# Optimization experiments

Measured on AMD Instinct MI355X. Metric: run time of the kernel, lower is better.

## Reference

```python
import jax, jax.numpy as jnp
import numpy as np

B, T, I, H, O = 1024, 512, 128, 256, 64


def setup_inputs() -> dict:
    key = jax.random.key(0)
    ks = jax.random.split(key, 12)
    def lin(k, shape, fan_in):
        return jax.random.uniform(k, shape, jnp.float32, -1.0, 1.0) / np.sqrt(fan_in)
    return {
        "x": jax.random.normal(ks[0], (B, T, I), jnp.float32),
        "h0": jnp.zeros((B, H), jnp.float32),
        # GRUCell params (gate order: r, z, n as in PyTorch)
        "W_ih": lin(ks[1], (3 * H, I), H),
        "b_ih": lin(ks[2], (3 * H,), H),
        "W_hh": lin(ks[3], (3 * H, H), H),
        "b_hh": lin(ks[4], (3 * H,), H),
        # input_transform Linear(I -> H)
        "Wt": lin(ks[5], (H, I), I),
        "bt": lin(ks[6], (H,), I),
        # output_proj Linear(H -> O)
        "Wo": lin(ks[7], (O, H), H),
        "bo": lin(ks[8], (O,), H),
        # gate_proj Linear(H -> O)
        "Wg": lin(ks[9], (O, H), H),
        "bg": lin(ks[10], (O,), H),
    }


def reference(x, h0, W_ih, b_ih, W_hh, b_hh, Wt, bt, Wo, bo, Wg, bg):
    # Precompute all input-side projections with big GEMMs (time-major for scan)
    xi = jnp.einsum("bti,gi->tbg", x, W_ih) + b_ih          # [T,B,3H]
    ti = jax.nn.silu(jnp.einsum("bti,hi->tbh", x, Wt) + bt)  # [T,B,H]

    def step(h, inp):
        xi_t, ti_t = inp
        hh = h @ W_hh.T + b_hh                               # [B,3H]
        xr, xz, xn = jnp.split(xi_t, 3, axis=-1)
        hr, hz, hn = jnp.split(hh, 3, axis=-1)
        r = jax.nn.sigmoid(xr + hr)
        z = jax.nn.sigmoid(xz + hz)
        n = jnp.tanh(xn + r * hn)
        h_new = (1.0 - z) * n + z * h
        proj = (h_new + ti_t) @ Wo.T + bo                    # [B,O]
        gate = jax.nn.sigmoid(h_new @ Wg.T + bg)             # [B,O]
        return h_new, proj * gate

    _, outs = jax.lax.scan(step, h0, (xi, ti))               # outs: [T,B,O]
    return jnp.mean(outs, axis=0)                            # [B,O]
```

## Files before the change

### kernel.cpp

```cpp
#include <hip/hip_runtime.h>
#include <hip/hip_bf16.h>


typedef __attribute__((ext_vector_type(8))) __bf16 bf16x8;
typedef __attribute__((ext_vector_type(4))) __bf16 bf16x4;
typedef __attribute__((ext_vector_type(4))) float f32x4;

#define MFMA(a, b, c) __builtin_amdgcn_mfma_f32_16x16x32_bf16(a, b, c, 0, 0, 0)

__device__ __forceinline__ float fsig(float v) {
  float e = __builtin_amdgcn_exp2f(v * -1.442695041f);
  return __builtin_amdgcn_rcpf(1.0f + e);
}
__device__ __forceinline__ float ftanh(float v) {
  float e = __builtin_amdgcn_exp2f(v * 2.885390082f);
  return 1.0f - 2.0f * __builtin_amdgcn_rcpf(1.0f + e);
}

#define O_WIN 0u
#define O_WHH 262144u
#define O_WO  655360u
#define O_WG  688128u
#define O_B1  720896u
#define O_H   724992u
#define O_ACC 1773568u
#define O_TIO 2035712u

__global__ void k1_prep(const float* __restrict__ Wih, const float* __restrict__ Wt,
                        const float* __restrict__ Whh, const float* __restrict__ Wo,
                        const float* __restrict__ Wg, const float* __restrict__ bih,
                        const float* __restrict__ bhh, const float* __restrict__ bt,
                        const float* __restrict__ h0, char* __restrict__ ws) {
  unsigned n = blockIdx.x * 256u + threadIdx.x;
  __bf16* win = (__bf16*)(ws + O_WIN);
  __bf16* whh = (__bf16*)(ws + O_WHH);
  __bf16* wo = (__bf16*)(ws + O_WO);
  __bf16* wg = (__bf16*)(ws + O_WG);
  float* b1 = (float*)(ws + O_B1);
  float* hb = (float*)(ws + O_H);
  float* ac = (float*)(ws + O_ACC);
  if (n < 98304u) win[n] = (__bf16)Wih[n];
  else if (n < 131072u) { unsigned i = n - 98304u; win[98304u + i] = (__bf16)Wt[i]; }
  else if (n < 327680u) { unsigned i = n - 131072u; whh[i] = (__bf16)Whh[i]; }
  else if (n < 344064u) { unsigned i = n - 327680u; wo[i] = (__bf16)Wo[i]; }
  else if (n < 360448u) { unsigned i = n - 344064u; wg[i] = (__bf16)Wg[i]; }
  else if (n < 361472u) {
    unsigned i = n - 360448u;
    float v = (i < 512u) ? (bih[i] + bhh[i]) : ((i < 768u) ? bih[i] : bt[i - 768u]);
    b1[i] = v;
  } else if (n < 623616u) { unsigned i = n - 361472u; hb[i] = h0[i]; }
  else if (n < 689152u) { unsigned i = n - 623616u; ac[i] = 0.0f; }
}

__global__ __launch_bounds__(256, 2) void k2_xi(
    const float* __restrict__ x, const __bf16* __restrict__ win,
    const float* __restrict__ b1, __bf16* __restrict__ xi, int t0, int tcbits) {
  extern __shared__ char sm2[];
  __bf16* Asm = (__bf16*)sm2;
  __bf16* Bsm = (__bf16*)(sm2 + 34816);
  const int tid = threadIdx.x;
  const int lane = tid & 63, wv = tid >> 6;
  const int m0 = blockIdx.x * 128;
  const int tcm = (1 << tcbits) - 1;
#pragma unroll
  for (int rnd = 0; rnd < 16; ++rnd) {
    int row = rnd * 8 + (tid >> 5);
    int cr = m0 + row;
    int bb = cr >> tcbits, tt = cr & tcm;
    const float* xr = x + ((size_t)bb * 512 + (size_t)(t0 + tt)) * 128 + (tid & 31) * 4;
    float4 v = *(const float4*)xr;
    bf16x4 b4 = {(__bf16)v.x, (__bf16)v.y, (__bf16)v.z, (__bf16)v.w};
    *(bf16x4*)&Asm[row * 136 + (tid & 31) * 4] = b4;
  }
  for (int nc = 0; nc < 6; ++nc) {
    __syncthreads();
#pragma unroll
    for (int rnd = 0; rnd < 8; ++rnd) {
      int rr = rnd * 16 + (tid >> 4);
      uint4 w4 = *(const uint4*)(win + (size_t)(nc * 128 + rr) * 128 + (tid & 15) * 8);
      *(uint4*)&Bsm[rr * 136 + (tid & 15) * 8] = w4;
    }
    __syncthreads();
    f32x4 zv = {0.f, 0.f, 0.f, 0.f};
    f32x4 acc[2][8];
#pragma unroll
    for (int mi = 0; mi < 2; ++mi)
#pragma unroll
      for (int nt = 0; nt < 8; ++nt) acc[mi][nt] = zv;
#pragma unroll
    for (int kt = 0; kt < 4; ++kt) {
      bf16x8 a0 = *(const bf16x8*)&Asm[(wv * 32 + (lane & 15)) * 136 + kt * 32 + (lane >> 4) * 8];
      bf16x8 a1 = *(const bf16x8*)&Asm[(wv * 32 + 16 + (lane & 15)) * 136 + kt * 32 + (lane >> 4) * 8];
#pragma unroll
      for (int nt = 0; nt < 8; ++nt) {
        bf16x8 b = *(const bf16x8*)&Bsm[(nt * 16 + (lane & 15)) * 136 + kt * 32 + (lane >> 4) * 8];
        acc[0][nt] = MFMA(a0, b, acc[0][nt]);
        acc[1][nt] = MFMA(a1, b, acc[1][nt]);
      }
    }
    __syncthreads();
#pragma unroll
    for (int nt = 0; nt < 8; ++nt) {
      float bv = b1[nc * 128 + nt * 16 + (lane & 15)];
#pragma unroll
      for (int mi = 0; mi < 2; ++mi)
#pragma unroll
        for (int r = 0; r < 4; ++r) {
          int rowb = wv * 32 + mi * 16 + (lane >> 4) * 4 + r;
          Bsm[rowb * 136 + nt * 16 + (lane & 15)] = (__bf16)(acc[mi][nt][r] + bv);
        }
    }
    __syncthreads();
#pragma unroll
    for (int rnd = 0; rnd < 8; ++rnd) {
      int row = rnd * 16 + (tid >> 4);
      int cr = m0 + row;
      int bb = cr >> tcbits, tt = cr & tcm;
      uint4 v = *(const uint4*)&Bsm[row * 136 + (tid & 15) * 8];
      *(uint4*)(xi + ((size_t)tt * 1024 + bb) * 768 + nc * 128 + (tid & 15) * 8) = v;
    }
  }
}

__global__ __launch_bounds__(256, 1) void k2_tio(
    const float* __restrict__ x, const __bf16* __restrict__ win,
    const __bf16* __restrict__ wo, const float* __restrict__ b1,
    const float* __restrict__ bo, __bf16* __restrict__ tio, int t0, int tcbits) {
  extern __shared__ char sm3[];
  __bf16* Asm = (__bf16*)sm3;
  __bf16* Bsm = (__bf16*)(sm3 + 34816);
  __bf16* Ti = (__bf16*)(sm3 + 69632);
  const int tid = threadIdx.x;
  const int lane = tid & 63, wv = tid >> 6;
  const int m0 = blockIdx.x * 128;
  const int tcm = (1 << tcbits) - 1;
#pragma unroll
  for (int rnd = 0; rnd < 16; ++rnd) {
    int row = rnd * 8 + (tid >> 5);
    int cr = m0 + row;
    int bb = cr >> tcbits, tt = cr & tcm;
    const float* xr = x + ((size_t)bb * 512 + (size_t)(t0 + tt)) * 128 + (tid & 31) * 4;
    float4 v = *(const float4*)xr;
    bf16x4 b4 = {(__bf16)v.x, (__bf16)v.y, (__bf16)v.z, (__bf16)v.w};
    *(bf16x4*)&Asm[row * 136 + (tid & 31) * 4] = b4;
  }
  for (int nc = 0; nc < 2; ++nc) {
    __syncthreads();
#pragma unroll
    for (int rnd = 0; rnd < 8; ++rnd) {
      int rr = rnd * 16 + (tid >> 4);
      uint4 w4 = *(const uint4*)(win + (size_t)(98304 / 128 + nc * 128 + rr) * 128 + (tid & 15) * 8);
      *(uint4*)&Bsm[rr * 136 + (tid & 15) * 8] = w4;
    }
    __syncthreads();
    f32x4 zv = {0.f, 0.f, 0.f, 0.f};
    f32x4 acc[2][8];
#pragma unroll
    for (int mi = 0; mi < 2; ++mi)
#pragma unroll
      for (int nt = 0; nt < 8; ++nt) acc[mi][nt] = zv;
#pragma unroll
    for (int kt = 0; kt < 4; ++kt) {
      bf16x8 a0 = *(const bf16x8*)&Asm[(wv * 32 + (lane & 15)) * 136 + kt * 32 + (lane >> 4) * 8];
      bf16x8 a1 = *(const bf16x8*)&Asm[(wv * 32 + 16 + (lane & 15)) * 136 + kt * 32 + (lane >> 4) * 8];
#pragma unroll
      for (int nt = 0; nt < 8; ++nt) {
        bf16x8 b = *(const bf16x8*)&Bsm[(nt * 16 + (lane & 15)) * 136 + kt * 32 + (lane >> 4) * 8];
        acc[0][nt] = MFMA(a0, b, acc[0][nt]);
        acc[1][nt] = MFMA(a1, b, acc[1][nt]);
      }
    }
#pragma unroll
    for (int nt = 0; nt < 8; ++nt) {
      float bv = b1[768 + nc * 128 + nt * 16 + (lane & 15)];
#pragma unroll
      for (int mi = 0; mi < 2; ++mi)
#pragma unroll
        for (int r = 0; r < 4; ++r) {
          int rowb = wv * 32 + mi * 16 + (lane >> 4) * 4 + r;
          float s = acc[mi][nt][r] + bv;
          s = s * __builtin_amdgcn_rcpf(1.0f + __builtin_amdgcn_exp2f(s * -1.442695041f));
          Ti[rowb * 264 + nc * 128 + nt * 16 + (lane & 15)] = (__bf16)s;
        }
    }
  }
  __syncthreads();
  for (int i = tid; i < 2048; i += 256) {
    int row = i >> 5;
    int c8 = (i & 31) * 8;
    *(uint4*)&Bsm[row * 264 + c8] = *(const uint4*)(wo + row * 256 + c8);
  }
  __syncthreads();
  f32x4 zv = {0.f, 0.f, 0.f, 0.f};
  f32x4 acc2[2][4];
#pragma unroll
  for (int mi = 0; mi < 2; ++mi)
#pragma unroll
    for (int nt = 0; nt < 4; ++nt) acc2[mi][nt] = zv;
#pragma unroll
  for (int kt = 0; kt < 8; ++kt) {
    bf16x8 a0 = *(const bf16x8*)&Ti[(wv * 32 + (lane & 15)) * 264 + kt * 32 + (lane >> 4) * 8];
    bf16x8 a1 = *(const bf16x8*)&Ti[(wv * 32 + 16 + (lane & 15)) * 264 + kt * 32 + (lane >> 4) * 8];
#pragma unroll
    for (int nt = 0; nt < 4; ++nt) {
      bf16x8 b = *(const bf16x8*)&Bsm[(nt * 16 + (lane & 15)) * 264 + kt * 32 + (lane >> 4) * 8];
      acc2[0][nt] = MFMA(a0, b, acc2[0][nt]);
      acc2[1][nt] = MFMA(a1, b, acc2[1][nt]);
    }
  }
#pragma unroll
  for (int nt = 0; nt < 4; ++nt) {
    int col = nt * 16 + (lane & 15);
    float bv = bo[col];
#pragma unroll
    for (int mi = 0; mi < 2; ++mi)
#pragma unroll
      for (int r = 0; r < 4; ++r) {
        int rowb = wv * 32 + mi * 16 + (lane >> 4) * 4 + r;
        int cr = m0 + rowb;
        int bb = cr >> tcbits, tt = cr & tcm;
        tio[((size_t)tt * 1024 + bb) * 64 + col] = (__bf16)(acc2[mi][nt][r] + bv);
      }
  }
}

__global__ __launch_bounds__(256, 1) void k3_rec(
    const __bf16* __restrict__ xi, const __bf16* __restrict__ tio,
    const __bf16* __restrict__ whh, const __bf16* __restrict__ wo,
    const __bf16* __restrict__ wg, const float* __restrict__ bhn,
    const float* __restrict__ bg, float* __restrict__ hbuf,
    float* __restrict__ accb, int TC) {
  extern __shared__ char sm[];
  __bf16* h_lds = (__bf16*)sm;
  float* pre = (float*)(sm + 8448);
  __bf16* xib = (__bf16*)(sm + 20736);
  __bf16* wow = (__bf16*)(sm + 34048);
  const int tid = threadIdx.x;
  const int lane = tid & 63, wv = tid >> 6;
  const int b0 = blockIdx.x * 4;
  const int gcp = lane * 4;

  bf16x8 wf[4][3][8];
#pragma unroll
  for (int p = 0; p < 4; ++p)
#pragma unroll
    for (int g = 0; g < 3; ++g)
#pragma unroll
      for (int kt = 0; kt < 8; ++kt) {
        int rowg = g * 256 + wv * 64 + p * 16 + (lane & 15);
        wf[p][g][kt] = *(const bf16x8*)(whh + (size_t)rowg * 256 + kt * 32 + (lane >> 4) * 8);
      }
  for (int i = tid; i < 4096; i += 256) {
    int row = i >> 5;
    int c8 = (i & 31) * 8;
    const __bf16* srcw = (row < 64) ? (wo + row * 256 + c8) : (wg + (row - 64) * 256 + c8);
    *(uint4*)&wow[row * 264 + c8] = *(const uint4*)srcw;
  }
  for (int i = tid; i < 2112; i += 256) ((unsigned*)h_lds)[i] = 0u;
  __syncthreads();
  float hreg[4];
  {
    f32x4 h4 = *(const f32x4*)(hbuf + (size_t)(b0 + wv) * 256 + gcp);
    hreg[0] = h4[0]; hreg[1] = h4[1]; hreg[2] = h4[2]; hreg[3] = h4[3];
    bf16x4 hb = {(__bf16)h4[0], (__bf16)h4[1], (__bf16)h4[2], (__bf16)h4[3]};
    *(bf16x4*)&h_lds[wv * 264 + gcp] = hb;
  }
  float bhnp[4];
#pragma unroll
  for (int p = 0; p < 4; ++p) bhnp[p] = bhn[wv * 64 + p * 16 + (lane & 15)];
  float bgv = bg[wv * 16 + (lane & 15)];
  float oacc[4] = {0.f, 0.f, 0.f, 0.f};
  if (lane < 16) {
#pragma unroll
    for (int r = 0; r < 4; ++r) oacc[r] = accb[(size_t)(b0 + r) * 64 + wv * 16 + lane];
  }
  {
    const uint2* s0 = (const uint2*)(xi + (size_t)b0 * 768);
    uint2* d0 = (uint2*)xib;
    d0[tid] = s0[tid]; d0[tid + 256] = s0[tid + 256]; d0[tid + 512] = s0[tid + 512];
    if (tid < 64) ((uint2*)(xib + 3072))[tid] = ((const uint2*)(tio + (size_t)b0 * 64))[tid];
  }
  __syncthreads();

#pragma unroll 1
  for (int t = 0; t < TC; ++t) {
    const int cur = t & 1, nxt = cur ^ 1;
    __bf16* xc = xib + cur * 3328;
    __bf16* xnb = xib + nxt * 3328;
    int tn = (t + 1 < TC) ? (t + 1) : t;
    uint2 pf0, pf1, pf2, pft;
    {
      const uint2* s = (const uint2*)(xi + ((size_t)tn * 1024 + b0) * 768);
      pf0 = s[tid]; pf1 = s[tid + 256]; pf2 = s[tid + 512];
      if (tid < 64) pft = ((const uint2*)(tio + ((size_t)tn * 1024 + b0) * 64))[tid];
    }
    bf16x8 afr[8];
#pragma unroll
    for (int kt = 0; kt < 8; ++kt)
      afr[kt] = *(const bf16x8*)&h_lds[(lane & 15) * 264 + kt * 32 + (lane >> 4) * 8];
#pragma unroll
    for (int p = 0; p < 4; ++p) {
      f32x4 ar = {0.f, 0.f, 0.f, 0.f}, az = {0.f, 0.f, 0.f, 0.f};
      f32x4 an = {bhnp[p], bhnp[p], bhnp[p], bhnp[p]};
#pragma unroll
      for (int kt = 0; kt < 8; ++kt) {
        ar = MFMA(afr[kt], wf[p][0][kt], ar);
        az = MFMA(afr[kt], wf[p][1][kt], az);
        an = MFMA(afr[kt], wf[p][2][kt], an);
      }
      if (lane < 16) {
        int col = wv * 64 + p * 16 + lane;
#pragma unroll
        for (int r = 0; r < 4; ++r) {
          pre[r * 256 + col] = ar[r];
          pre[1024 + r * 256 + col] = az[r];
          pre[2048 + r * 256 + col] = an[r];
        }
      }
    }
    __syncthreads();
    {
      f32x4 hr = *(const f32x4*)&pre[wv * 256 + gcp];
      f32x4 hz = *(const f32x4*)&pre[1024 + wv * 256 + gcp];
      f32x4 hn = *(const f32x4*)&pre[2048 + wv * 256 + gcp];
      bf16x4 xr4 = *(const bf16x4*)&xc[wv * 768 + gcp];
      bf16x4 xz4 = *(const bf16x4*)&xc[wv * 768 + 256 + gcp];
      bf16x4 xn4 = *(const bf16x4*)&xc[wv * 768 + 512 + gcp];
#pragma unroll
      for (int j = 0; j < 4; ++j) {
        float r = fsig((float)xr4[j] + hr[j]);
        float z = fsig((float)xz4[j] + hz[j]);
        float n = ftanh((float)xn4[j] + r * hn[j]);
        hreg[j] = n + z * (hreg[j] - n);
      }
      bf16x4 hb = {(__bf16)hreg[0], (__bf16)hreg[1], (__bf16)hreg[2], (__bf16)hreg[3]};
      *(bf16x4*)&h_lds[wv * 264 + gcp] = hb;
    }
    {
      uint2* d = (uint2*)xnb;
      d[tid] = pf0; d[tid + 256] = pf1; d[tid + 512] = pf2;
      if (tid < 64) ((uint2*)(xnb + 3072))[tid] = pft;
    }
    __syncthreads();
    {
      bf16x8 af2[8];
#pragma unroll
      for (int kt = 0; kt < 8; ++kt)
        af2[kt] = *(const bf16x8*)&h_lds[(lane & 15) * 264 + kt * 32 + (lane >> 4) * 8];
      f32x4 po = {0.f, 0.f, 0.f, 0.f};
      f32x4 pg = {bgv, bgv, bgv, bgv};
#pragma unroll
      for (int kt = 0; kt < 8; ++kt) {
        bf16x8 bfo = *(const bf16x8*)&wow[(wv * 16 + (lane & 15)) * 264 + kt * 32 + (lane >> 4) * 8];
        bf16x8 bfg = *(const bf16x8*)&wow[(64 + wv * 16 + (lane & 15)) * 264 + kt * 32 + (lane >> 4) * 8];
        po = MFMA(af2[kt], bfo, po);
        pg = MFMA(af2[kt], bfg, pg);
      }
      if (lane < 16) {
#pragma unroll
        for (int r = 0; r < 4; ++r) {
          float tv = (float)xc[3072 + r * 64 + wv * 16 + lane];
          float pov = po[r] + tv;
          float gv = fsig(pg[r]);
          oacc[r] += pov * gv;
        }
      }
    }
  }
  {
    f32x4 h4 = {hreg[0], hreg[1], hreg[2], hreg[3]};
    *(f32x4*)(hbuf + (size_t)(b0 + wv) * 256 + gcp) = h4;
  }
  if (lane < 16) {
#pragma unroll
    for (int r = 0; r < 4; ++r) accb[(size_t)(b0 + r) * 64 + wv * 16 + lane] = oacc[r];
  }
}

__global__ void k4_out(const float* __restrict__ accb, float* __restrict__ out) {
  int i = blockIdx.x * 256 + threadIdx.x;
  out[i] = accb[i] * (1.0f / 512.0f);
}

extern "C" void kernel_launch(void* const* d_in, const int* in_sizes, int n_in,
                              void* d_out, int out_size, void* d_ws, size_t ws_size,
                              hipStream_t stream) {
  const float* x = (const float*)d_in[0];
  const float* h0 = (const float*)d_in[1];
  const float* Wih = (const float*)d_in[2];
  const float* bih = (const float*)d_in[3];
  const float* Whh = (const float*)d_in[4];
  const float* bhh = (const float*)d_in[5];
  const float* Wt = (const float*)d_in[6];
  const float* bt = (const float*)d_in[7];
  const float* Wo = (const float*)d_in[8];
  const float* bo = (const float*)d_in[9];
  const float* Wg = (const float*)d_in[10];
  const float* bg = (const float*)d_in[11];
  float* out = (float*)d_out;
  char* ws = (char*)d_ws;

  int TC = 512;
  while (TC > 1 && (2035712ull + (size_t)TC * 1703936ull) > ws_size) TC >>= 1;
  int tcbits = 0;
  while ((1 << tcbits) != TC) ++tcbits;

  __bf16* win = (__bf16*)(ws + O_WIN);
  __bf16* whhb = (__bf16*)(ws + O_WHH);
  __bf16* wob = (__bf16*)(ws + O_WO);
  __bf16* wgb = (__bf16*)(ws + O_WG);
  float* b1 = (float*)(ws + O_B1);
  float* hbuf = (float*)(ws + O_H);
  float* accb = (float*)(ws + O_ACC);
  __bf16* tioc = (__bf16*)(ws + O_TIO);
  __bf16* xic = (__bf16*)(ws + O_TIO + (size_t)TC * 131072u);

  (void)hipFuncSetAttribute((const void*)k2_xi, hipFuncAttributeMaxDynamicSharedMemorySize, 69632);
  (void)hipFuncSetAttribute((const void*)k2_tio, hipFuncAttributeMaxDynamicSharedMemorySize, 137216);
  (void)hipFuncSetAttribute((const void*)k3_rec, hipFuncAttributeMaxDynamicSharedMemorySize, 101632);

  k1_prep<<<2692, 256, 0, stream>>>(Wih, Wt, Whh, Wo, Wg, bih, bhh, bt, h0, ws);
  int nch = 512 / TC;
  for (int c = 0; c < nch; ++c) {
    int t0 = c * TC;
    k2_xi<<<8 * TC, 256, 69632, stream>>>(x, win, b1, xic, t0, tcbits);
    k2_tio<<<8 * TC, 256, 137216, stream>>>(x, win, wob, b1, bo, tioc, t0, tcbits);
    k3_rec<<<256, 256, 101632, stream>>>(xic, tioc, whhb, wob, wgb, bhh + 512, bg, hbuf, accb, TC);
  }
  k4_out<<<256, 256, 0, stream>>>(accb, out);
}
```

Before: 2.223 ms.

## Split recurrent hidden dimension across four blocks with cross-block flag sync

The recurrence kernel now assigns 16 batch rows to a group of four blocks, each owning a quarter of the hidden columns. The blocks exchange bf16 hidden states through a double-buffered global buffer, using per-group atomic counters with spin-waits. Output and gate projections are split across waves and reduced through LDS. The projection is deferred one step so it overlaps the next step's GRU work. The xi and tio staging layouts are retiled to suit the new per-block access pattern. This raises per-step MFMA parallelism and halves the per-block weight footprint. The cost is a global synchronisation round-trip every timestep, and a dependence on all 256 blocks being co-resident.

Result: slower. 7.694 ms (+246.1%).

```diff
diff --git a/kernel.cpp b/kernel.cpp
--- a/kernel.cpp
+++ b/kernel.cpp
@@ -4,6 +4,7 @@
 
 typedef __attribute__((ext_vector_type(8))) __bf16 bf16x8;
 typedef __attribute__((ext_vector_type(4))) __bf16 bf16x4;
+typedef __attribute__((ext_vector_type(2))) __bf16 bf16x2;
 typedef __attribute__((ext_vector_type(4))) float f32x4;
 
 #define MFMA(a, b, c) __builtin_amdgcn_mfma_f32_16x16x32_bf16(a, b, c, 0, 0, 0)
@@ -24,7 +25,9 @@
 #define O_B1  720896u
 #define O_H   724992u
 #define O_ACC 1773568u
-#define O_TIO 2035712u
+#define O_HX  2035712u
+#define O_CTR 3084288u
+#define O_TIO 3088384u
 
 __global__ void k1_prep(const float* __restrict__ Wih, const float* __restrict__ Wt,
                         const float* __restrict__ Whh, const float* __restrict__ Wo,
@@ -39,6 +42,7 @@
   float* b1 = (float*)(ws + O_B1);
   float* hb = (float*)(ws + O_H);
   float* ac = (float*)(ws + O_ACC);
+  unsigned* ct = (unsigned*)(ws + O_CTR);
   if (n < 98304u) win[n] = (__bf16)Wih[n];
   else if (n < 131072u) { unsigned i = n - 98304u; win[98304u + i] = (__bf16)Wt[i]; }
   else if (n < 327680u) { unsigned i = n - 131072u; whh[i] = (__bf16)Whh[i]; }
@@ -50,6 +54,7 @@
     b1[i] = v;
   } else if (n < 623616u) { unsigned i = n - 361472u; hb[i] = h0[i]; }
   else if (n < 689152u) { unsigned i = n - 623616u; ac[i] = 0.0f; }
+  else if (n < 690176u) { unsigned i = n - 689152u; ct[i] = 0u; }
 }
 
 __global__ __launch_bounds__(256, 2) void k2_xi(
@@ -117,7 +122,11 @@
       int cr = m0 + row;
       int bb = cr >> tcbits, tt = cr & tcm;
       uint4 v = *(const uint4*)&Bsm[row * 136 + (tid & 15) * 8];
-      *(uint4*)(xi + ((size_t)tt * 1024 + bb) * 768 + nc * 128 + (tid & 15) * 8) = v;
+      int col = nc * 128 + (tid & 15) * 8;
+      int g = col >> 8, gc = col & 255;
+      size_t dst = ((((size_t)tt * 64 + (bb >> 4)) * 4 + (gc >> 6)) * 16 + (bb & 15)) * 192
+                   + g * 64 + (gc & 63);
+      *(uint4*)(xi + dst) = v;
     }
   }
 }
@@ -219,7 +228,9 @@
         int rowb = wv * 32 + mi * 16 + (lane >> 4) * 4 + r;
         int cr = m0 + rowb;
         int bb = cr >> tcbits, tt = cr & tcm;
-        tio[((size_t)tt * 1024 + bb) * 64 + col] = (__bf16)(acc2[mi][nt][r] + bv);
+        size_t dst = ((((size_t)tt * 64 + (bb >> 4)) * 4 + (col >> 4)) * 16 + (bb & 15)) * 16
+                     + (col & 15);
+        tio[dst] = (__bf16)(acc2[mi][nt][r] + bv);
       }
   }
 }
@@ -228,153 +239,207 @@
     const __bf16* __restrict__ xi, const __bf16* __restrict__ tio,
     const __bf16* __restrict__ whh, const __bf16* __restrict__ wo,
     const __bf16* __restrict__ wg, const float* __restrict__ bhn,
-    const float* __restrict__ bg, float* __restrict__ hbuf,
-    float* __restrict__ accb, int TC) {
+    const float* __restrict__ bg, float* __restrict__ hbufg,
+    float* __restrict__ accb, __bf16* __restrict__ hx,
+    unsigned* __restrict__ ctr, int TC, int t0) {
   extern __shared__ char sm[];
-  __bf16* h_lds = (__bf16*)sm;
-  float* pre = (float*)(sm + 8448);
-  __bf16* xib = (__bf16*)(sm + 20736);
-  __bf16* wow = (__bf16*)(sm + 34048);
+  __bf16* hb = (__bf16*)sm;
+  float* pjb = (float*)(sm + 16896);
   const int tid = threadIdx.x;
   const int lane = tid & 63, wv = tid >> 6;
-  const int b0 = blockIdx.x * 4;
-  const int gcp = lane * 4;
-
-  bf16x8 wf[4][3][8];
-#pragma unroll
-  for (int p = 0; p < 4; ++p)
-#pragma unroll
-    for (int g = 0; g < 3; ++g)
-#pragma unroll
-      for (int kt = 0; kt < 8; ++kt) {
-        int rowg = g * 256 + wv * 64 + p * 16 + (lane & 15);
-        wf[p][g][kt] = *(const bf16x8*)(whh + (size_t)rowg * 256 + kt * 32 + (lane >> 4) * 8);
-      }
-  for (int i = tid; i < 4096; i += 256) {
-    int row = i >> 5;
-    int c8 = (i & 31) * 8;
-    const __bf16* srcw = (row < 64) ? (wo + row * 256 + c8) : (wg + (row - 64) * 256 + c8);
-    *(uint4*)&wow[row * 264 + c8] = *(const uint4*)srcw;
-  }
-  for (int i = tid; i < 2112; i += 256) ((unsigned*)h_lds)[i] = 0u;
-  __syncthreads();
+  const int l15 = lane & 15, lg = lane >> 4;
+  const int rg = blockIdx.x & 63, cg = blockIdx.x >> 6;
+  unsigned* myctr = ctr + rg * 16;
+
+  bf16x8 wf[3][8];
+#pragma unroll
+  for (int g = 0; g < 3; ++g)
+#pragma unroll
+    for (int kt = 0; kt < 8; ++kt)
+      wf[g][kt] = *(const bf16x8*)(whh + (size_t)(g * 256 + cg * 64 + wv * 16 + l15) * 256
+                                   + kt * 32 + lg * 8);
+  bf16x8 wpo[2], wpg[2];
+#pragma unroll
+  for (int j = 0; j < 2; ++j) {
+    wpo[j] = *(const bf16x8*)(wo + (size_t)(cg * 16 + l15) * 256 + (2 * wv + j) * 32 + lg * 8);
+    wpg[j] = *(const bf16x8*)(wg + (size_t)(cg * 16 + l15) * 256 + (2 * wv + j) * 32 + lg * 8);
+  }
+  const int hcol = cg * 64 + wv * 16 + lg * 4;
+  float bhnp[4];
+#pragma unroll
+  for (int r = 0; r < 4; ++r) bhnp[r] = bhn[hcol + r];
+  const int cb = tid >> 4, cc = tid & 15;
+  const float bgv = bg[cg * 16 + cc];
+  float oacc = accb[((size_t)rg * 16 + cb) * 64 + cg * 16 + cc];
+
   float hreg[4];
   {
-    f32x4 h4 = *(const f32x4*)(hbuf + (size_t)(b0 + wv) * 256 + gcp);
-    hreg[0] = h4[0]; hreg[1] = h4[1]; hreg[2] = h4[2]; hreg[3] = h4[3];
-    bf16x4 hb = {(__bf16)h4[0], (__bf16)h4[1], (__bf16)h4[2], (__bf16)h4[3]};
-    *(bf16x4*)&h_lds[wv * 264 + gcp] = hb;
-  }
-  float bhnp[4];
-#pragma unroll
-  for (int p = 0; p < 4; ++p) bhnp[p] = bhn[wv * 64 + p * 16 + (lane & 15)];
-  float bgv = bg[wv * 16 + (lane & 15)];
-  float oacc[4] = {0.f, 0.f, 0.f, 0.f};
-  if (lane < 16) {
-#pragma unroll
-    for (int r = 0; r < 4; ++r) oacc[r] = accb[(size_t)(b0 + r) * 64 + wv * 16 + lane];
-  }
+    const float* hp = hbufg + ((size_t)rg * 16 + l15) * 256 + hcol;
+#pragma unroll
+    for (int r = 0; r < 4; ++r) hreg[r] = hp[r];
+  }
+  if (t0 == 0) {
+#pragma unroll
+    for (int j = 0; j < 4; ++j) {
+      f32x4 v = *(const f32x4*)(hbufg + ((size_t)rg * 16 + cb) * 256 + cc * 16 + j * 4);
+      bf16x4 b4 = {(__bf16)v[0], (__bf16)v[1], (__bf16)v[2], (__bf16)v[3]};
+      *(bf16x4*)&hb[cb * 264 + cc * 16 + j * 4] = b4;
+    }
+  }
+  bf16x4 xiN[3];
   {
-    const uint2* s0 = (const uint2*)(xi + (size_t)b0 * 768);
-    uint2* d0 = (uint2*)xib;
-    d0[tid] = s0[tid]; d0[tid + 256] = s0[tid + 256]; d0[tid + 512] = s0[tid + 512];
-    if (tid < 64) ((uint2*)(xib + 3072))[tid] = ((const uint2*)(tio + (size_t)b0 * 64))[tid];
-  }
+    const __bf16* xs = xi + ((size_t)rg * 4 + cg) * 3072;
+#pragma unroll
+    for (int g = 0; g < 3; ++g)
+      xiN[g] = *(const bf16x4*)(xs + l15 * 192 + g * 64 + wv * 16 + lg * 4);
+  }
+  float tioB = 0.f;
   __syncthreads();
 
 #pragma unroll 1
   for (int t = 0; t < TC; ++t) {
+    const int s = t0 + t;
     const int cur = t & 1, nxt = cur ^ 1;
-    __bf16* xc = xib + cur * 3328;
-    __bf16* xnb = xib + nxt * 3328;
-    int tn = (t + 1 < TC) ? (t + 1) : t;
-    uint2 pf0, pf1, pf2, pft;
+    if (s > 0) {
+      if (tid == 0) {
+#pragma unroll
+        for (int q = 0; q < 4; ++q) {
+          if (q == cg) continue;
+          while (__hip_atomic_load(&myctr[q], __ATOMIC_RELAXED, __HIP_MEMORY_SCOPE_AGENT)
+                 < (unsigned)s)
+            __builtin_amdgcn_s_sleep(2);
+        }
+#pragma unroll
+        for (int q = 0; q < 4; ++q)
+          if (q != cg)
+            (void)__hip_atomic_load(&myctr[q], __ATOMIC_ACQUIRE, __HIP_MEMORY_SCOPE_AGENT);
+      }
+      __syncthreads();
+      const __bf16* hsl = hx + (size_t)((s - 1) & 1) * 262144;
+#pragma unroll
+      for (int c4 = 0; c4 < 4; ++c4) {
+        unsigned long long v = __hip_atomic_load(
+            (unsigned long long*)(hsl + ((size_t)rg * 4 + c4) * 1024 + cb * 64 + cc * 4),
+            __ATOMIC_RELAXED, __HIP_MEMORY_SCOPE_AGENT);
+        *(unsigned long long*)&hb[cur * 4224 + cb * 264 + c4 * 64 + cc * 4] = v;
+      }
+    }
+    bf16x4 xiC[3];
+#pragma unroll
+    for (int g = 0; g < 3; ++g) xiC[g] = xiN[g];
     {
-      const uint2* s = (const uint2*)(xi + ((size_t)tn * 1024 + b0) * 768);
-      pf0 = s[tid]; pf1 = s[tid + 256]; pf2 = s[tid + 512];
-      if (tid < 64) pft = ((const uint2*)(tio + ((size_t)tn * 1024 + b0) * 64))[tid];
-    }
+      int tn = (t + 1 < TC) ? t + 1 : t;
+      const __bf16* xs = xi + (((size_t)tn * 64 + rg) * 4 + cg) * 3072;
+#pragma unroll
+      for (int g = 0; g < 3; ++g)
+        xiN[g] = *(const bf16x4*)(xs + l15 * 192 + g * 64 + wv * 16 + lg * 4);
+    }
+    float tioC = (float)tio[(((size_t)t * 64 + rg) * 4 + cg) * 256 + cb * 16 + cc];
+    __syncthreads();
     bf16x8 afr[8];
 #pragma unroll
     for (int kt = 0; kt < 8; ++kt)
-      afr[kt] = *(const bf16x8*)&h_lds[(lane & 15) * 264 + kt * 32 + (lane >> 4) * 8];
-#pragma unroll
-    for (int p = 0; p < 4; ++p) {
-      f32x4 ar = {0.f, 0.f, 0.f, 0.f}, az = {0.f, 0.f, 0.f, 0.f};
-      f32x4 an = {bhnp[p], bhnp[p], bhnp[p], bhnp[p]};
-#pragma unroll
-      for (int kt = 0; kt < 8; ++kt) {
-        ar = MFMA(afr[kt], wf[p][0][kt], ar);
-        az = MFMA(afr[kt], wf[p][1][kt], az);
-        an = MFMA(afr[kt], wf[p][2][kt], an);
-      }
-      if (lane < 16) {
-        int col = wv * 64 + p * 16 + lane;
-#pragma unroll
-        for (int r = 0; r < 4; ++r) {
-          pre[r * 256 + col] = ar[r];
-          pre[1024 + r * 256 + col] = az[r];
-          pre[2048 + r * 256 + col] = an[r];
-        }
-      }
-    }
-    __syncthreads();
+      afr[kt] = *(const bf16x8*)&hb[cur * 4224 + l15 * 264 + kt * 32 + lg * 8];
+    f32x4 ar = {0.f, 0.f, 0.f, 0.f}, az = {0.f, 0.f, 0.f, 0.f}, an = {0.f, 0.f, 0.f, 0.f};
+#pragma unroll
+    for (int kt = 0; kt < 8; ++kt) {
+      ar = MFMA(wf[0][kt], afr[kt], ar);
+      az = MFMA(wf[1][kt], afr[kt], az);
+      an = MFMA(wf[2][kt], afr[kt], an);
+    }
+    f32x4 po = {0.f, 0.f, 0.f, 0.f}, pg4 = {0.f, 0.f, 0.f, 0.f};
+#pragma unroll
+    for (int j = 0; j < 2; ++j) {
+      po = MFMA(wpo[j], afr[2 * wv + j], po);
+      pg4 = MFMA(wpg[j], afr[2 * wv + j], pg4);
+    }
+    *(f32x4*)&pjb[(cur * 8 + wv * 2 + 0) * 256 + l15 * 16 + lg * 4] = po;
+    *(f32x4*)&pjb[(cur * 8 + wv * 2 + 1) * 256 + l15 * 16 + lg * 4] = pg4;
     {
-      f32x4 hr = *(const f32x4*)&pre[wv * 256 + gcp];
-      f32x4 hz = *(const f32x4*)&pre[1024 + wv * 256 + gcp];
-      f32x4 hn = *(const f32x4*)&pre[2048 + wv * 256 + gcp];
-      bf16x4 xr4 = *(const bf16x4*)&xc[wv * 768 + gcp];
-      bf16x4 xz4 = *(const bf16x4*)&xc[wv * 768 + 256 + gcp];
-      bf16x4 xn4 = *(const bf16x4*)&xc[wv * 768 + 512 + gcp];
-#pragma unroll
-      for (int j = 0; j < 4; ++j) {
-        float r = fsig((float)xr4[j] + hr[j]);
-        float z = fsig((float)xz4[j] + hz[j]);
-        float n = ftanh((float)xn4[j] + r * hn[j]);
-        hreg[j] = n + z * (hreg[j] - n);
-      }
-      bf16x4 hb = {(__bf16)hreg[0], (__bf16)hreg[1], (__bf16)hreg[2], (__bf16)hreg[3]};
-      *(bf16x4*)&h_lds[wv * 264 + gcp] = hb;
-    }
-    {
-      uint2* d = (uint2*)xnb;
-      d[tid] = pf0; d[tid + 256] = pf1; d[tid + 512] = pf2;
-      if (tid < 64) ((uint2*)(xnb + 3072))[tid] = pft;
-    }
-    __syncthreads();
-    {
-      bf16x8 af2[8];
-#pragma unroll
-      for (int kt = 0; kt < 8; ++kt)
-        af2[kt] = *(const bf16x8*)&h_lds[(lane & 15) * 264 + kt * 32 + (lane >> 4) * 8];
-      f32x4 po = {0.f, 0.f, 0.f, 0.f};
-      f32x4 pg = {bgv, bgv, bgv, bgv};
-#pragma unroll
-      for (int kt = 0; kt < 8; ++kt) {
-        bf16x8 bfo = *(const bf16x8*)&wow[(wv * 16 + (lane & 15)) * 264 + kt * 32 + (lane >> 4) * 8];
-        bf16x8 bfg = *(const bf16x8*)&wow[(64 + wv * 16 + (lane & 15)) * 264 + kt * 32 + (lane >> 4) * 8];
-        po = MFMA(af2[kt], bfo, po);
-        pg = MFMA(af2[kt], bfg, pg);
-      }
-      if (lane < 16) {
-#pragma unroll
-        for (int r = 0; r < 4; ++r) {
-          float tv = (float)xc[3072 + r * 64 + wv * 16 + lane];
-          float pov = po[r] + tv;
-          float gv = fsig(pg[r]);
-          oacc[r] += pov * gv;
-        }
-      }
-    }
+#pragma unroll
+      for (int r = 0; r < 4; ++r) {
+        float r_ = fsig((float)xiC[0][r] + ar[r]);
+        float z_ = fsig((float)xiC[1][r] + az[r]);
+        float n_ = ftanh((float)xiC[2][r] + r_ * (an[r] + bhnp[r]));
+        hreg[r] = n_ + z_ * (hreg[r] - n_);
+      }
+      bf16x4 h4 = {(__bf16)hreg[0], (__bf16)hreg[1], (__bf16)hreg[2], (__bf16)hreg[3]};
+      *(bf16x4*)&hb[nxt * 4224 + l15 * 264 + hcol] = h4;
+      unsigned long long uv;
+      __builtin_memcpy(&uv, &h4, 8);
+      __hip_atomic_store(
+          (unsigned long long*)(hx + (size_t)(s & 1) * 262144 + ((size_t)rg * 4 + cg) * 1024
+                                + l15 * 64 + wv * 16 + lg * 4),
+          uv, __ATOMIC_RELAXED, __HIP_MEMORY_SCOPE_AGENT);
+    }
+    __syncthreads();
+    if (tid == 0)
+      __hip_atomic_store(&myctr[cg], (unsigned)(s + 1), __ATOMIC_RELEASE,
+                         __HIP_MEMORY_SCOPE_AGENT);
+    if (t >= 1) {
+      float p_o = 0.f, p_g = bgv;
+#pragma unroll
+      for (int w2 = 0; w2 < 4; ++w2) {
+        p_o += pjb[(cur * 8 + w2 * 2 + 0) * 256 + cb * 16 + cc];
+        p_g += pjb[(cur * 8 + w2 * 2 + 1) * 256 + cb * 16 + cc];
+      }
+      oacc += (p_o + tioB) * fsig(p_g);
+    }
+    tioB = tioC;
   }
   {
-    f32x4 h4 = {hreg[0], hreg[1], hreg[2], hreg[3]};
-    *(f32x4*)(hbuf + (size_t)(b0 + wv) * 256 + gcp) = h4;
-  }
-  if (lane < 16) {
-#pragma unroll
-    for (int r = 0; r < 4; ++r) accb[(size_t)(b0 + r) * 64 + wv * 16 + lane] = oacc[r];
-  }
+    const int s = t0 + TC;
+    const int cur = TC & 1;
+    if (tid == 0) {
+#pragma unroll
+      for (int q = 0; q < 4; ++q) {
+        if (q == cg) continue;
+        while (__hip_atomic_load(&myctr[q], __ATOMIC_RELAXED, __HIP_MEMORY_SCOPE_AGENT)
+               < (unsigned)s)
+          __builtin_amdgcn_s_sleep(2);
+      }
+#pragma unroll
+      for (int q = 0; q < 4; ++q)
+        if (q != cg)
+          (void)__hip_atomic_load(&myctr[q], __ATOMIC_ACQUIRE, __HIP_MEMORY_SCOPE_AGENT);
+    }
+    __syncthreads();
+    const __bf16* hsl = hx + (size_t)((s - 1) & 1) * 262144;
+#pragma unroll
+    for (int c4 = 0; c4 < 4; ++c4) {
+      unsigned long long v = __hip_atomic_load(
+          (unsigned long long*)(hsl + ((size_t)rg * 4 + c4) * 1024 + cb * 64 + cc * 4),
+          __ATOMIC_RELAXED, __HIP_MEMORY_SCOPE_AGENT);
+      *(unsigned long long*)&hb[cur * 4224 + cb * 264 + c4 * 64 + cc * 4] = v;
+    }
+    __syncthreads();
+    bf16x8 afr[8];
+#pragma unroll
+    for (int kt = 0; kt < 8; ++kt)
+      afr[kt] = *(const bf16x8*)&hb[cur * 4224 + l15 * 264 + kt * 32 + lg * 8];
+    f32x4 po = {0.f, 0.f, 0.f, 0.f}, pg4 = {0.f, 0.f, 0.f, 0.f};
+#pragma unroll
+    for (int j = 0; j < 2; ++j) {
+      po = MFMA(wpo[j], afr[2 * wv + j], po);
+      pg4 = MFMA(wpg[j], afr[2 * wv + j], pg4);
+    }
+    *(f32x4*)&pjb[(cur * 8 + wv * 2 + 0) * 256 + l15 * 16 + lg * 4] = po;
+    *(f32x4*)&pjb[(cur * 8 + wv * 2 + 1) * 256 + l15 * 16 + lg * 4] = pg4;
+    __syncthreads();
+    float p_o = 0.f, p_g = bgv;
+#pragma unroll
+    for (int w2 = 0; w2 < 4; ++w2) {
+      p_o += pjb[(cur * 8 + w2 * 2 + 0) * 256 + cb * 16 + cc];
+      p_g += pjb[(cur * 8 + w2 * 2 + 1) * 256 + cb * 16 + cc];
+    }
+    oacc += (p_o + tioB) * fsig(p_g);
+  }
+  {
+    float* hp = hbufg + ((size_t)rg * 16 + l15) * 256 + hcol;
+#pragma unroll
+    for (int r = 0; r < 4; ++r) hp[r] = hreg[r];
+  }
+  accb[((size_t)rg * 16 + cb) * 64 + cg * 16 + cc] = oacc;
 }
 
 __global__ void k4_out(const float* __restrict__ accb, float* __restrict__ out) {
@@ -401,7 +466,7 @@
   char* ws = (char*)d_ws;
 
   int TC = 512;
-  while (TC > 1 && (2035712ull + (size_t)TC * 1703936ull) > ws_size) TC >>= 1;
+  while (TC > 1 && (3088384ull + (size_t)TC * 1703936ull) > ws_size) TC >>= 1;
   int tcbits = 0;
   while ((1 << tcbits) != TC) ++tcbits;
 
@@ -412,20 +477,23 @@
   float* b1 = (float*)(ws + O_B1);
   float* hbuf = (float*)(ws + O_H);
   float* accb = (float*)(ws + O_ACC);
+  __bf16* hxb = (__bf16*)(ws + O_HX);
+  unsigned* ctrb = (unsigned*)(ws + O_CTR);
   __bf16* tioc = (__bf16*)(ws + O_TIO);
   __bf16* xic = (__bf16*)(ws + O_TIO + (size_t)TC * 131072u);
 
   (void)hipFuncSetAttribute((const void*)k2_xi, hipFuncAttributeMaxDynamicSharedMemorySize, 69632);
   (void)hipFuncSetAttribute((const void*)k2_tio, hipFuncAttributeMaxDynamicSharedMemorySize, 137216);
-  (void)hipFuncSetAttribute((const void*)k3_rec, hipFuncAttributeMaxDynamicSharedMemorySize, 101632);
-
-  k1_prep<<<2692, 256, 0, stream>>>(Wih, Wt, Whh, Wo, Wg, bih, bhh, bt, h0, ws);
+  (void)hipFuncSetAttribute((const void*)k3_rec, hipFuncAttributeMaxDynamicSharedMemorySize, 33280);
+
+  k1_prep<<<2696, 256, 0, stream>>>(Wih, Wt, Whh, Wo, Wg, bih, bhh, bt, h0, ws);
   int nch = 512 / TC;
   for (int c = 0; c < nch; ++c) {
     int t0 = c * TC;
     k2_xi<<<8 * TC, 256, 69632, stream>>>(x, win, b1, xic, t0, tcbits);
     k2_tio<<<8 * TC, 256, 137216, stream>>>(x, win, wob, b1, bo, tioc, t0, tcbits);
-    k3_rec<<<256, 256, 101632, stream>>>(xic, tioc, whhb, wob, wgb, bhh + 512, bg, hbuf, accb, TC);
+    k3_rec<<<256, 256, 33280, stream>>>(xic, tioc, whhb, wob, wgb, bhh + 512, bg, hbuf,
+                                        accb, hxb, ctrb, TC, t0);
   }
   k4_out<<<256, 256, 0, stream>>>(accb, out);
 }
```
